# Optimization experiments

Hardware: AMD Instinct MI355X
Metric: run time of the kernel (lower is better)

## Reference

```python
import jax, jax.numpy as jnp
import numpy as np

M, N, L, D = 2048, 256, 128, 300  # context len, n entities, query len, d2
DROOT = float(np.sqrt(D))


def setup_inputs() -> dict:
    key = jax.random.key(0)
    ks = jax.random.split(key, 16)
    s = 0.05
    return {
        "context_emb": jax.random.normal(ks[0], (M, D), jnp.float32),
        "query_emb": jax.random.normal(ks[1], (L, D), jnp.float32),
        "bin_M": (jax.random.uniform(ks[2], (M, N)) < 0.02).astype(jnp.float32),  # sparse token->entity incidence
        "adj": (jax.random.uniform(ks[3], (N, N)) < 0.05).astype(jnp.float32),    # entity graph adjacency
        "V": jax.random.normal(ks[4], (D, 2 * D), jnp.float32) * s,
        "U": jax.random.normal(ks[5], (D, 2 * D), jnp.float32) * s,
        "b": jax.random.normal(ks[6], (D,), jnp.float32) * s,
        "W": jax.random.normal(ks[7], (2 * D,), jnp.float32) * s,
        "w_att": jax.random.normal(ks[8], (3, D), jnp.float32) * s,   # BiDAF trilinear weights (w_c, w_q, w_cq)
        "b_att": jax.random.normal(ks[9], (3,), jnp.float32) * s,
        "W_red": jax.random.normal(ks[10], (D, 4 * D), jnp.float32) * s,  # BiDAF reduction Linear(4*d2 -> d2)
        "b_red": jax.random.normal(ks[11], (D,), jnp.float32) * s,
        "W_ih": jax.random.normal(ks[12], (4 * D, 2 * D), jnp.float32) * s,  # LSTM input weights
        "b_ih": jax.random.normal(ks[13], (4 * D,), jnp.float32) * s,
        "b_hh": jax.random.normal(ks[14], (4 * D,), jnp.float32) * s,
        "passes": 1,
    }


def _tok2ent(context, bin_M):
    # avg_pool1d over full M divides by M (zeros of unmasked tokens included) -> exact mean/M
    mean = (bin_M.T @ context) / M                       # (N, D)
    masked = context[:, None, :] * bin_M[:, :, None]     # (M, N, D) dominant intermediate
    mx = masked.max(axis=0)                              # (N, D) max includes the zeros, as in torch
    return jnp.concatenate([mean, mx], axis=-1)          # (N, 2D)


def _graph_attention(ent, query, adj, V, U, b, W):
    q = query.mean(axis=0)                               # avg-pooled query (D,)
    gammas = ((q @ V) @ ent.T) / DROOT                   # (N,)
    E = jax.nn.sigmoid(gammas)[:, None] * ent            # soft entity mask, (N, 2D)
    hidden = E @ U.T + b                                 # (N, D)
    a_i = hidden @ W[:D]                                 # (N,) source half of W.[h_i;h_j]
    c_j = hidden @ W[D:]                                 # (N,)
    betas = jnp.where(adj > 0, jax.nn.leaky_relu(a_i[:, None] + c_j[None, :]), 0.0)
    # original exponentiates ALL betas incl. the zeros of non-edges -> plain softmax over axis 1
    alphas = jax.nn.softmax(betas, axis=1)               # (N, N)
    # E_t[i] = relu( sum_{j: adj[i,j]} alphas[j,i] * hidden[j] )
    return jax.nn.relu((adj * alphas.T) @ hidden)        # (N, D)


def _bidaf(ent, query, w_att, b_att, W_red, b_red):
    # trilinear similarity S[l, n] = w_c.q_l + w_q.e_n + w_cq.(q_l * e_n)
    S = (query @ w_att[0] + b_att[0])[:, None] \
        + (ent @ w_att[1] + b_att[1])[None, :] \
        + (query * w_att[2]) @ ent.T + b_att[2]          # (L, N)
    c2q = jax.nn.softmax(S, axis=1) @ ent                # (L, D)
    q2c = jax.nn.softmax(S.max(axis=1), axis=0) @ query  # (D,)
    x = jnp.concatenate([query, c2q, query * c2q, query * q2c[None, :]], axis=-1)  # (L, 4D)
    return x @ W_red.T + b_red                           # (L, D)


def _graph2doc(context, ent, bin_M, W_ih, b_ih, b_hh):
    x = jnp.concatenate([context, bin_M @ ent], axis=-1)  # (M, 2D)
    # nn.LSTM fed (seq=1, batch=M, 2D) from zero state == one LSTM-cell step per token
    gates = x @ W_ih.T + (b_ih + b_hh)                    # (M, 4D), torch gate order i,f,g,o
    i, f, g, o = jnp.split(gates, 4, axis=-1)
    c = jax.nn.sigmoid(i) * jnp.tanh(g)                   # f*c0 vanishes since c0 = 0
    return jax.nn.sigmoid(o) * jnp.tanh(c)                # (M, D)


def reference(context_emb, query_emb, bin_M, adj, V, U, b, W, w_att, b_att,
              W_red, b_red, W_ih, b_ih, b_hh, passes):
    ctx, qry = context_emb, query_emb
    for _ in range(passes):
        ent = _tok2ent(ctx, bin_M)                        # (N, 2D)
        E_t = _graph_attention(ent, qry, adj, V, U, b, W)  # (N, D)
        qry = _bidaf(E_t, qry, w_att, b_att, W_red, b_red)  # (L, D)
        ctx = _graph2doc(ctx, E_t, bin_M, W_ih, b_ih, b_hh)  # (M, D)
    return ctx, qry
```

## Files before the change

### kernel.cpp

```cpp
#include <hip/hip_runtime.h>
#include <hip/hip_bf16.h>
#include <math.h>

#define MM 2048
#define NN 256
#define LL 128
#define DD 300
#define D2 600
#define D4 1200
#define DROOT 17.320508075688775f

#define KP 608
#define NP 960
#define GM 64
#define GDT 64
#define GK 32

typedef __attribute__((ext_vector_type(8))) short bf16x8;
typedef __attribute__((ext_vector_type(4))) float f32x4;

__device__ __forceinline__ float sigmoidf_(float x) { return 1.f / (1.f + expf(-x)); }

__device__ __forceinline__ ushort f2bf(float v) {
    union { float f; unsigned u; } x; x.f = v;
    unsigned r = x.u + 0x7fffu + ((x.u >> 16) & 1u);
    return (ushort)(r >> 16);
}

__device__ __forceinline__ float dot4_(float4 a, float4 b) {
    return a.x * b.x + a.y * b.y + a.z * b.z + a.w * b.w;
}

__device__ __forceinline__ float bfdot8(uint4 u, float4 x0, float4 x1) {
    union { unsigned v; float f; } a, b;
    float s = 0.f;
    a.v = u.x << 16; b.v = u.x & 0xffff0000u; s += a.f * x0.x; s += b.f * x0.y;
    a.v = u.y << 16; b.v = u.y & 0xffff0000u; s += a.f * x0.z; s += b.f * x0.w;
    a.v = u.z << 16; b.v = u.z & 0xffff0000u; s += a.f * x1.x; s += b.f * x1.y;
    a.v = u.w << 16; b.v = u.w & 0xffff0000u; s += a.f * x1.z; s += b.f * x1.w;
    return s;
}

__device__ __forceinline__ float wave_red_sum(float v) {
    for (int off = 32; off; off >>= 1) v += __shfl_down(v, off);
    return v;
}

__global__ __launch_bounds__(256) void k_prep(const float* __restrict__ binM,
                                              const float* __restrict__ Wih,
                                              const float* __restrict__ U,
                                              const float* __restrict__ Wred,
                                              const float* __restrict__ query,
                                              const float* __restrict__ V,
                                              ushort* __restrict__ Wb,
                                              ushort* __restrict__ Ub,
                                              ushort* __restrict__ Wredb,
                                              unsigned* __restrict__ binMbits,
                                              float* __restrict__ qVp) {
    __shared__ float qp2[2][75];
    __shared__ float qp_s[75];
    int r = blockIdx.x, t = threadIdx.x;
    if (r < NP) {
        int s = r / 320, dd = r % 320;
        bool valid = (dd < DD);
        int src = (s == 0) ? dd : ((s == 1) ? 600 + dd : 900 + dd);
        for (int e = t; e < KP; e += 256) {
            float v = (valid && e < D2) ? Wih[(size_t)src * D2 + e] : 0.f;
            Wb[(size_t)r * KP + e] = f2bf(v);
        }
    } else if (r < NP + DD) {
        int rr = r - NP;
        for (int e = t; e < D2; e += 256) Ub[(size_t)rr * D2 + e] = f2bf(U[(size_t)rr * D2 + e]);
    } else if (r < NP + 2 * DD) {
        int rr = r - NP - DD;
        for (int e = t; e < D4; e += 256) Wredb[(size_t)rr * D4 + e] = f2bf(Wred[(size_t)rr * D4 + e]);
    } else if (r < NP + 2 * DD + 12) {
        int q = r - NP - 2 * DD;
        int kb = q >> 2, sl = q & 3;
        int dbase = sl * 75;
        if (t < 150) {
            int dd = t % 75, half = t / 75;
            float s = 0.f;
            #pragma unroll 8
            for (int l = half * 64; l < half * 64 + 64; ++l) s += query[l * DD + dbase + dd];
            qp2[half][dd] = s;
        }
        __syncthreads();
        if (t < 75) qp_s[t] = (qp2[0][t] + qp2[1][t]) * (1.f / LL);
        __syncthreads();
        int k = kb * 256 + t;
        if (k < D2) {
            float acc = 0.f;
            #pragma unroll 5
            for (int i = 0; i < 75; ++i) acc += qp_s[i] * V[(size_t)(dbase + i) * D2 + k];
            qVp[sl * D2 + k] = acc;
        }
    } else {
        int blk = r - NP - 2 * DD - 12;
        int m0 = blk * 32;
        unsigned mask = 0u;
        #pragma unroll 8
        for (int i = 0; i < 32; ++i) {
            if (binM[(size_t)(m0 + i) * NN + t] != 0.f) mask |= (1u << i);
        }
        binMbits[(size_t)t * 64 + blk] = mask;
    }
}

__global__ __launch_bounds__(960) void k_hidden(const float* __restrict__ ctx,
                                                const unsigned* __restrict__ binMbits,
                                                const float* __restrict__ qVp,
                                                const ushort* __restrict__ Ub,
                                                const float* __restrict__ bvec,
                                                const float* __restrict__ W,
                                                float* __restrict__ hidden,
                                                float* __restrict__ a_i,
                                                float* __restrict__ c_j) {
    __shared__ int lst[MM];
    __shared__ int wbase_s[65];
    __shared__ alignas(16) float e_s[D2];
    __shared__ float h_s[DD];
    __shared__ float red[2][16];
    __shared__ float sig_s;
    int n = blockIdx.x, t = threadIdx.x, wv = t >> 6, lane = t & 63;
    unsigned mword = (t < 64) ? binMbits[(size_t)n * 64 + t] : 0u;
    if (t < 64) wbase_s[t] = (int)__popc(mword);
    __syncthreads();
    if (t == 0) {
        int s = 0;
        for (int w = 0; w < 64; ++w) { int c = wbase_s[w]; wbase_s[w] = s; s += c; }
        wbase_s[64] = s;
    }
    __syncthreads();
    if (t < 64) {
        int base = wbase_s[t];
        unsigned x = mword;
        while (x) {
            int b = __ffs((int)x) - 1;
            lst[base++] = t * 32 + b;
            x &= x - 1;
        }
    }
    __syncthreads();
    int total = wbase_s[64];
    if (t < DD) {
        float sum = 0.f, mx = 0.f;
        int i = 0;
        for (; i + 4 <= total; i += 4) {
            float v0 = ctx[(size_t)lst[i] * DD + t];
            float v1 = ctx[(size_t)lst[i + 1] * DD + t];
            float v2 = ctx[(size_t)lst[i + 2] * DD + t];
            float v3 = ctx[(size_t)lst[i + 3] * DD + t];
            sum += v0; mx = fmaxf(mx, v0);
            sum += v1; mx = fmaxf(mx, v1);
            sum += v2; mx = fmaxf(mx, v2);
            sum += v3; mx = fmaxf(mx, v3);
        }
        for (; i < total; ++i) {
            float v = ctx[(size_t)lst[i] * DD + t];
            sum += v; mx = fmaxf(mx, v);
        }
        e_s[t]      = sum * (1.f / MM);
        e_s[DD + t] = mx;
    }
    __syncthreads();
    float part = 0.f;
    if (t < D2) part = e_s[t] * (qVp[t] + qVp[D2 + t] + qVp[2 * D2 + t] + qVp[3 * D2 + t]);
    part = wave_red_sum(part);
    if (lane == 0) red[0][wv] = part;
    __syncthreads();
    if (t == 0) {
        float s = 0.f;
        for (int w = 0; w < 15; ++w) s += red[0][w];
        sig_s = sigmoidf_(s / DROOT);
    }
    __syncthreads();
    float sg = sig_s;
    const float4* e4 = (const float4*)e_s;
    float4 ex0 = e4[2 * lane], ex1 = e4[2 * lane + 1];
    float4 ex2 = {0.f, 0.f, 0.f, 0.f}, ex3 = {0.f, 0.f, 0.f, 0.f};
    if (lane < 11) { ex2 = e4[128 + 2 * lane]; ex3 = e4[129 + 2 * lane]; }
    #pragma unroll 4
    for (int i = 0; i < 20; ++i) {
        int d = wv * 20 + i;
        const uint4* u4 = (const uint4*)(Ub + (size_t)d * D2);
        float p2 = bfdot8(u4[lane], ex0, ex1);
        if (lane < 11) p2 += bfdot8(u4[64 + lane], ex2, ex3);
        p2 = wave_red_sum(p2);
        if (lane == 0) {
            float h = sg * p2 + bvec[d];
            h_s[d] = h;
            hidden[n * DD + d] = h;
        }
    }
    __syncthreads();
    float wa = 0.f, wc = 0.f;
    if (t < DD) { float h = h_s[t]; wa = h * W[t]; wc = h * W[DD + t]; }
    wa = wave_red_sum(wa); wc = wave_red_sum(wc);
    if (lane == 0) { red[0][wv] = wa; red[1][wv] = wc; }
    __syncthreads();
    if (t == 0) {
        float A = 0.f, C = 0.f;
        for (int w = 0; w < 15; ++w) { A += red[0][w]; C += red[1][w]; }
        a_i[n] = A; c_j[n] = C;
    }
}

__global__ __launch_bounds__(256) void k_alphas(const float* __restrict__ adj,
                                                const float* __restrict__ ai,
                                                const float* __restrict__ cj,
                                                float* __restrict__ alphas) {
    __shared__ float red[4];
    __shared__ float bc[2];
    int i = blockIdx.x, j = threadIdx.x;
    float beta = 0.f;
    if (adj[i * NN + j] > 0.f) {
        float v = ai[i] + cj[j];
        beta = (v > 0.f) ? v : 0.01f * v;
    }
    float wm = beta;
    for (int off = 32; off; off >>= 1) wm = fmaxf(wm, __shfl_down(wm, off));
    if ((j & 63) == 0) red[j >> 6] = wm;
    __syncthreads();
    if (j == 0) bc[0] = fmaxf(fmaxf(red[0], red[1]), fmaxf(red[2], red[3]));
    __syncthreads();
    float e = expf(beta - bc[0]);
    float ws_ = e;
    for (int off = 32; off; off >>= 1) ws_ += __shfl_down(ws_, off);
    __syncthreads();
    if ((j & 63) == 0) red[j >> 6] = ws_;
    __syncthreads();
    if (j == 0) bc[1] = 1.f / (red[0] + red[1] + red[2] + red[3]);
    __syncthreads();
    alphas[i * NN + j] = e * bc[1];
}

__global__ __launch_bounds__(960) void k_Et(const float* __restrict__ adj,
                                            const float* __restrict__ alphas,
                                            const float* __restrict__ hidden,
                                            const float* __restrict__ w_att,
                                            const float* __restrict__ b_att,
                                            float* __restrict__ Et,
                                            float* __restrict__ EtT,
                                            float* __restrict__ ce) {
    __shared__ float w_s[NN];
    __shared__ float epart[3][DD];
    __shared__ float red[16];
    int i = blockIdx.x, t = threadIdx.x, wv = t >> 6;
    if (t < NN) w_s[t] = adj[i * NN + t] * alphas[t * NN + i];
    __syncthreads();
    int d = t % 320, sl = t / 320;
    int j0 = sl * 86, j1 = (sl == 2) ? NN : (j0 + 86);
    if (d < DD) {
        float acc = 0.f;
        #pragma unroll 2
        for (int j = j0; j < j1; ++j) acc += w_s[j] * hidden[(size_t)j * DD + d];
        epart[sl][d] = acc;
    }
    __syncthreads();
    float pv = 0.f;
    if (t < DD) {
        float etv = fmaxf(epart[0][t] + epart[1][t] + epart[2][t], 0.f);
        Et[i * DD + t] = etv;
        EtT[(size_t)t * NN + i] = etv;
        pv = etv * w_att[DD + t];
    }
    pv = wave_red_sum(pv);
    if ((t & 63) == 0) red[wv] = pv;
    __syncthreads();
    if (t == 0) {
        float s = 0.f;
        for (int w = 0; w < 15; ++w) s += red[w];
        ce[i] = s + b_att[1];
    }
}

__global__ __launch_bounds__(1024) void k_Bmid(const float* __restrict__ query,
                                               const float* __restrict__ Et,
                                               const float* __restrict__ EtT,
                                               const float* __restrict__ w_att,
                                               const float* __restrict__ b_att,
                                               const float* __restrict__ ce,
                                               const float* __restrict__ ctx,
                                               const float* __restrict__ binM,
                                               float* __restrict__ rowmax,
                                               float* __restrict__ c2qg,
                                               ushort* __restrict__ Xb) {
    __shared__ alignas(16) float qw[DD];
    __shared__ float s_row[NN];
    __shared__ alignas(16) float p_s[NN];
    __shared__ float red[16];
    __shared__ float cql_s, rmax_s, invs;
    __shared__ int lst4[4][NN];
    __shared__ int wcnt4[4][4];
    __shared__ int tot4[4];
    int t = threadIdx.x, wv = t >> 6, lane = t & 63;
    if (blockIdx.x < LL) {
        int l = blockIdx.x;
        float part = 0.f;
        if (t < DD) {
            float qv = query[l * DD + t];
            qw[t] = qv * w_att[2 * DD + t];
            part = qv * w_att[t];
        }
        part = wave_red_sum(part);
        if (lane == 0) red[wv] = part;
        __syncthreads();
        if (t == 0) {
            float s = 0.f;
            for (int w = 0; w < 16; ++w) s += red[w];
            cql_s = s + b_att[0];
        }
        __syncthreads();
        const float4* q4 = (const float4*)qw;
        float4 qb0 = q4[lane];
        float4 qb1 = (lane < 11) ? q4[64 + lane] : float4{0.f, 0.f, 0.f, 0.f};
        float wmax = -1e30f;
        #pragma unroll 4
        for (int i = 0; i < 16; ++i) {
            int n = wv * 16 + i;
            const float4* e4 = (const float4*)(Et + (size_t)n * DD);
            float4 a0 = e4[lane];
            float p2 = dot4_(a0, qb0);
            if (lane < 11) { float4 a1 = e4[64 + lane]; p2 += dot4_(a1, qb1); }
            p2 = wave_red_sum(p2);
            if (lane == 0) {
                float val = cql_s + ce[n] + p2 + b_att[2];
                s_row[n] = val;
                wmax = fmaxf(wmax, val);
            }
        }
        if (lane == 0) red[wv] = wmax;
        __syncthreads();
        if (t == 0) {
            float m = red[0];
            for (int w = 1; w < 16; ++w) m = fmaxf(m, red[w]);
            rmax_s = m;
            rowmax[l] = m;
        }
        __syncthreads();
        float e = 0.f;
        if (t < NN) e = expf(s_row[t] - rmax_s);
        float v = wave_red_sum(e);
        if (lane == 0) red[wv] = v;
        __syncthreads();
        if (t == 0) {
            float s = 0.f;
            for (int w = 0; w < 16; ++w) s += red[w];
            invs = 1.f / s;
        }
        __syncthreads();
        if (t < NN) p_s[t] = e * invs;
        __syncthreads();
        if (wv < 15) {
            const float4* p4 = (const float4*)p_s;
            float4 pb = p4[lane];
            #pragma unroll 4
            for (int i = 0; i < 20; ++i) {
                int d = wv * 20 + i;
                float4 a = ((const float4*)(EtT + (size_t)d * NN))[lane];
                float p2 = wave_red_sum(dot4_(a, pb));
                if (lane == 0) c2qg[l * DD + d] = p2;
            }
        }
    } else {
        int g = t >> 8, tt = t & 255;
        int w2 = tt >> 6;
        int m = (blockIdx.x - LL) * 4 + g;
        float b = binM[(size_t)m * NN + tt];
        unsigned long long mask = __ballot(b != 0.f);
        int prefix = __popcll(mask & ((1ull << lane) - 1ull));
        if (lane == 0) wcnt4[g][w2] = (int)__popcll(mask);
        __syncthreads();
        int wbase = 0;
        for (int w = 0; w < w2; ++w) wbase += wcnt4[g][w];
        if (b != 0.f) lst4[g][wbase + prefix] = tt;
        if (tt == 0) tot4[g] = wcnt4[g][0] + wcnt4[g][1] + wcnt4[g][2] + wcnt4[g][3];
        __syncthreads();
        int total = tot4[g];
        if (tt < 8) Xb[(size_t)m * KP + D2 + tt] = 0;
        for (int d = tt; d < DD; d += 256) {
            Xb[(size_t)m * KP + d] = f2bf(ctx[(size_t)m * DD + d]);
            float s = 0.f;
            for (int i = 0; i < total; ++i) s += Et[(size_t)lst4[g][i] * DD + d];
            Xb[(size_t)m * KP + DD + d] = f2bf(s);
        }
    }
}

__global__ __launch_bounds__(320) void k_tail(const float* __restrict__ c2qg,
                                              const float* __restrict__ rowmax,
                                              const float* __restrict__ query,
                                              const ushort* __restrict__ Wredb,
                                              const float* __restrict__ bred,
                                              const ushort* __restrict__ Xb,
                                              const ushort* __restrict__ Wb,
                                              const float* __restrict__ bih,
                                              const float* __restrict__ bhh,
                                              float* __restrict__ outq,
                                              float* __restrict__ outc) {
    __shared__ float pq[LL];
    __shared__ float q2c_s[DD];
    __shared__ alignas(16) float xs[D4];
    __shared__ float red[5];
    __shared__ float bc2[2];
    __shared__ ushort As[GM * GK];
    __shared__ ushort Bs[3][GDT * GK];
    int t = threadIdx.x, wv = t >> 6, lane = t & 63;
    if (blockIdx.x < 3 * LL) {
        int s = blockIdx.x / LL, l = blockIdx.x % LL;
        float v = (t < LL) ? rowmax[t] : -1e30f;
        float wm = v;
        for (int off = 32; off; off >>= 1) wm = fmaxf(wm, __shfl_down(wm, off));
        if (lane == 0) red[wv] = wm;
        __syncthreads();
        if (t == 0) {
            float m = red[0];
            for (int w = 1; w < 5; ++w) m = fmaxf(m, red[w]);
            bc2[0] = m;
        }
        __syncthreads();
        float e = (t < LL) ? expf(v - bc2[0]) : 0.f;
        float ws_ = wave_red_sum(e);
        __syncthreads();
        if (lane == 0) red[wv] = ws_;
        __syncthreads();
        if (t == 0) {
            float sm = 0.f;
            for (int w = 0; w < 5; ++w) sm += red[w];
            bc2[1] = 1.f / sm;
        }
        __syncthreads();
        if (t < LL) pq[t] = e * bc2[1];
        __syncthreads();
        if (t < DD) {
            float s2 = 0.f;
            #pragma unroll 4
            for (int l2 = 0; l2 < LL; ++l2) s2 += pq[l2] * query[l2 * DD + t];
            q2c_s[t] = s2;
        }
        __syncthreads();
        if (t < DD) {
            float c = c2qg[l * DD + t];
            float qv = query[l * DD + t];
            xs[t] = qv; xs[DD + t] = c; xs[2 * DD + t] = qv * c; xs[3 * DD + t] = qv * q2c_s[t];
        }
        __syncthreads();
        const float4* x4 = (const float4*)xs;
        float4 xb0 = x4[2 * lane], xb1 = x4[2 * lane + 1];
        float4 xb2 = x4[128 + 2 * lane], xb3 = x4[129 + 2 * lane];
        float4 xb4 = {0.f, 0.f, 0.f, 0.f}, xb5 = {0.f, 0.f, 0.f, 0.f};
        if (lane < 22) { xb4 = x4[256 + 2 * lane]; xb5 = x4[257 + 2 * lane]; }
        int d0 = s * 100 + wv * 20;
        #pragma unroll 2
        for (int i = 0; i < 20; ++i) {
            int d = d0 + i;
            const uint4* w4 = (const uint4*)(Wredb + (size_t)d * D4);
            float p2 = bfdot8(w4[lane], xb0, xb1) + bfdot8(w4[64 + lane], xb2, xb3);
            if (lane < 22) p2 += bfdot8(w4[128 + lane], xb4, xb5);
            p2 = wave_red_sum(p2);
            if (lane == 0) outq[l * DD + d] = bred[d] + p2;
        }
    } else {
        int g = blockIdx.x - 3 * LL;
        int m0 = (g & 31) * GM, d0 = (g >> 5) * GDT;
        int tid = t;
        int wm = wv >> 1, wn = wv & 1;
        int l15 = lane & 15, l4 = lane >> 4;
        f32x4 acc[3][2][2] = {};
        int srow = tid >> 2, kslot = tid & 3;
        int sidx = srow * GK + ((kslot ^ ((srow >> 1) & 3)) << 3);
        for (int k0 = 0; k0 < KP; k0 += GK) {
            if (tid < 256) {
                uint4 va = *(const uint4*)(Xb + (size_t)(m0 + srow) * KP + k0 + kslot * 8);
                *(uint4*)(As + sidx) = va;
                #pragma unroll
                for (int s = 0; s < 3; ++s) {
                    uint4 vb = *(const uint4*)(Wb + (size_t)(s * 320 + d0 + srow) * KP + k0 + kslot * 8);
                    *(uint4*)(Bs[s] + sidx) = vb;
                }
            }
            __syncthreads();
            if (tid < 256) {
                bf16x8 af[2], bfr[3][2];
                #pragma unroll
                for (int mi = 0; mi < 2; ++mi) {
                    int row = wm * 32 + mi * 16 + l15;
                    af[mi] = *(const bf16x8*)(As + row * GK + ((l4 ^ ((row >> 1) & 3)) << 3));
                }
                #pragma unroll
                for (int s = 0; s < 3; ++s)
                    #pragma unroll
                    for (int ni = 0; ni < 2; ++ni) {
                        int row = wn * 32 + ni * 16 + l15;
                        bfr[s][ni] = *(const bf16x8*)(Bs[s] + row * GK + ((l4 ^ ((row >> 1) & 3)) << 3));
                    }
                #pragma unroll
                for (int s = 0; s < 3; ++s)
                    #pragma unroll
                    for (int mi = 0; mi < 2; ++mi)
                        #pragma unroll
                        for (int ni = 0; ni < 2; ++ni)
                            acc[s][mi][ni] = __builtin_amdgcn_mfma_f32_16x16x32_bf16(af[mi], bfr[s][ni], acc[s][mi][ni], 0, 0, 0);
            }
            __syncthreads();
        }
        if (tid < 256) {
            #pragma unroll
            for (int mi = 0; mi < 2; ++mi) {
                #pragma unroll
                for (int ni = 0; ni < 2; ++ni) {
                    int d = d0 + wn * 32 + ni * 16 + l15;
                    if (d < DD) {
                        float bi = bih[d] + bhh[d];
                        float bg = bih[2 * DD + d] + bhh[2 * DD + d];
                        float bo = bih[3 * DD + d] + bhh[3 * DD + d];
                        int mrow = m0 + wm * 32 + mi * 16 + l4 * 4;
                        #pragma unroll
                        for (int r2 = 0; r2 < 4; ++r2) {
                            float gi = acc[0][mi][ni][r2] + bi;
                            float gg = acc[1][mi][ni][r2] + bg;
                            float go = acc[2][mi][ni][r2] + bo;
                            float c = sigmoidf_(gi) * tanhf(gg);
                            outc[(size_t)(mrow + r2) * DD + d] = sigmoidf_(go) * tanhf(c);
                        }
                    }
                }
            }
        }
    }
}

extern "C" void kernel_launch(void* const* d_in, const int* in_sizes, int n_in,
                              void* d_out, int out_size, void* d_ws, size_t ws_size,
                              hipStream_t stream) {
    const float* context = (const float*)d_in[0];
    const float* query   = (const float*)d_in[1];
    const float* binM    = (const float*)d_in[2];
    const float* adj     = (const float*)d_in[3];
    const float* V       = (const float*)d_in[4];
    const float* U       = (const float*)d_in[5];
    const float* bvec    = (const float*)d_in[6];
    const float* W       = (const float*)d_in[7];
    const float* w_att   = (const float*)d_in[8];
    const float* b_att   = (const float*)d_in[9];
    const float* W_red   = (const float*)d_in[10];
    const float* b_red   = (const float*)d_in[11];
    const float* W_ih    = (const float*)d_in[12];
    const float* b_ih    = (const float*)d_in[13];
    const float* b_hh    = (const float*)d_in[14];

    float* ws = (float*)d_ws;
    float* qVp    = ws;
    float* hidden = qVp    + 2400;
    float* a_i    = hidden + 76800;
    float* c_j    = a_i    + 256;
    float* alphas = c_j    + 256;
    float* Et     = alphas + 65536;
    float* EtT    = Et     + 76800;
    float* ce     = EtT    + 76800;
    float* rmax   = ce     + 256;
    float* c2qg   = rmax   + 128;
    unsigned* binMbits = (unsigned*)(c2qg + 38400);
    ushort* Xb    = (ushort*)(binMbits + (size_t)NN * 64);
    ushort* Wb    = Xb + (size_t)MM * KP;
    ushort* Ub    = Wb + (size_t)NP * KP;
    ushort* Wredb = Ub + (size_t)DD * D2;

    float* outc = (float*)d_out;
    float* outq = (float*)d_out + MM * DD;

    hipLaunchKernelGGL(k_prep,    dim3(NP + 2 * DD + 12 + 64), dim3(256), 0, stream,
                       binM, W_ih, U, W_red, query, V, Wb, Ub, Wredb, binMbits, qVp);
    hipLaunchKernelGGL(k_hidden,  dim3(NN), dim3(960), 0, stream, context, binMbits, qVp, Ub, bvec, W, hidden, a_i, c_j);
    hipLaunchKernelGGL(k_alphas,  dim3(NN), dim3(256), 0, stream, adj, a_i, c_j, alphas);
    hipLaunchKernelGGL(k_Et,      dim3(NN), dim3(960), 0, stream, adj, alphas, hidden, w_att, b_att, Et, EtT, ce);
    hipLaunchKernelGGL(k_Bmid,    dim3(LL + MM / 4), dim3(1024), 0, stream,
                       query, Et, EtT, w_att, b_att, ce, context, binM, rmax, c2qg, Xb);
    hipLaunchKernelGGL(k_tail,    dim3(3 * LL + 160), dim3(320), 0, stream,
                       c2qg, rmax, query, Wredb, b_red, Xb, Wb, b_ih, b_hh, outq, outc);
}
```

Baseline: 115.5 us.

## Fuse post-prep kernels into one cooperative persistent kernel with grid syncs

Replaces the hidden, alphas, Et, Bmid and tail kernels with a single cooperative kernel of 256 blocks of 1024 threads that moves between phases with grid.sync(). The alphas matrix is no longer materialized; per-row softmax statistics (mstat, rinv) are stored instead. The LSTM GEMM tiles are regrouped as four 256-thread sub-tiles per block. This removes several kernel launch gaps and intermediate round trips. In exchange the grid is capped at 256 blocks, uses a large shared-memory footprint, and pays grid-wide barrier costs. Phases that previously used more blocks may lose parallelism.

```diff
diff --git a/kernel.cpp b/kernel.cpp
--- a/kernel.cpp
+++ b/kernel.cpp
@@ -1,6 +1,9 @@
 #include <hip/hip_runtime.h>
+#include <hip/hip_cooperative_groups.h>
 #include <hip/hip_bf16.h>
 #include <math.h>
+
+namespace cg = cooperative_groups;
 
 #define MM 2048
 #define NN 256
@@ -107,331 +110,334 @@
     }
 }
 
-__global__ __launch_bounds__(960) void k_hidden(const float* __restrict__ ctx,
-                                                const unsigned* __restrict__ binMbits,
-                                                const float* __restrict__ qVp,
-                                                const ushort* __restrict__ Ub,
-                                                const float* __restrict__ bvec,
-                                                const float* __restrict__ W,
-                                                float* __restrict__ hidden,
-                                                float* __restrict__ a_i,
-                                                float* __restrict__ c_j) {
+__global__ __launch_bounds__(1024) void k_main(const float* __restrict__ ctx,
+                                               const float* __restrict__ binM,
+                                               const float* __restrict__ adj,
+                                               const float* __restrict__ query,
+                                               const float* __restrict__ qVp,
+                                               const unsigned* __restrict__ binMbits,
+                                               const ushort* __restrict__ Ub,
+                                               const ushort* __restrict__ Wredb,
+                                               const ushort* __restrict__ Wb,
+                                               const float* __restrict__ bvec,
+                                               const float* __restrict__ W,
+                                               const float* __restrict__ w_att,
+                                               const float* __restrict__ b_att,
+                                               const float* __restrict__ bred,
+                                               const float* __restrict__ bih,
+                                               const float* __restrict__ bhh,
+                                               float* __restrict__ hidden,
+                                               float* __restrict__ a_i,
+                                               float* __restrict__ c_j,
+                                               float* __restrict__ mstat,
+                                               float* __restrict__ rinv,
+                                               float* __restrict__ Et,
+                                               float* __restrict__ EtT,
+                                               float* __restrict__ ce,
+                                               float* __restrict__ rmax,
+                                               float* __restrict__ c2qg,
+                                               ushort* __restrict__ Xb,
+                                               float* __restrict__ outq,
+                                               float* __restrict__ outc) {
+    cg::grid_group grid = cg::this_grid();
     __shared__ int lst[MM];
     __shared__ int wbase_s[65];
     __shared__ alignas(16) float e_s[D2];
     __shared__ float h_s[DD];
-    __shared__ float red[2][16];
-    __shared__ float sig_s;
-    int n = blockIdx.x, t = threadIdx.x, wv = t >> 6, lane = t & 63;
-    unsigned mword = (t < 64) ? binMbits[(size_t)n * 64 + t] : 0u;
-    if (t < 64) wbase_s[t] = (int)__popc(mword);
-    __syncthreads();
-    if (t == 0) {
-        int s = 0;
-        for (int w = 0; w < 64; ++w) { int c = wbase_s[w]; wbase_s[w] = s; s += c; }
-        wbase_s[64] = s;
-    }
-    __syncthreads();
-    if (t < 64) {
-        int base = wbase_s[t];
-        unsigned x = mword;
-        while (x) {
-            int b = __ffs((int)x) - 1;
-            lst[base++] = t * 32 + b;
-            x &= x - 1;
-        }
-    }
-    __syncthreads();
-    int total = wbase_s[64];
-    if (t < DD) {
-        float sum = 0.f, mx = 0.f;
-        int i = 0;
-        for (; i + 4 <= total; i += 4) {
-            float v0 = ctx[(size_t)lst[i] * DD + t];
-            float v1 = ctx[(size_t)lst[i + 1] * DD + t];
-            float v2 = ctx[(size_t)lst[i + 2] * DD + t];
-            float v3 = ctx[(size_t)lst[i + 3] * DD + t];
-            sum += v0; mx = fmaxf(mx, v0);
-            sum += v1; mx = fmaxf(mx, v1);
-            sum += v2; mx = fmaxf(mx, v2);
-            sum += v3; mx = fmaxf(mx, v3);
-        }
-        for (; i < total; ++i) {
-            float v = ctx[(size_t)lst[i] * DD + t];
-            sum += v; mx = fmaxf(mx, v);
-        }
-        e_s[t]      = sum * (1.f / MM);
-        e_s[DD + t] = mx;
-    }
-    __syncthreads();
-    float part = 0.f;
-    if (t < D2) part = e_s[t] * (qVp[t] + qVp[D2 + t] + qVp[2 * D2 + t] + qVp[3 * D2 + t]);
-    part = wave_red_sum(part);
-    if (lane == 0) red[0][wv] = part;
-    __syncthreads();
-    if (t == 0) {
-        float s = 0.f;
-        for (int w = 0; w < 15; ++w) s += red[0][w];
-        sig_s = sigmoidf_(s / DROOT);
-    }
-    __syncthreads();
-    float sg = sig_s;
-    const float4* e4 = (const float4*)e_s;
-    float4 ex0 = e4[2 * lane], ex1 = e4[2 * lane + 1];
-    float4 ex2 = {0.f, 0.f, 0.f, 0.f}, ex3 = {0.f, 0.f, 0.f, 0.f};
-    if (lane < 11) { ex2 = e4[128 + 2 * lane]; ex3 = e4[129 + 2 * lane]; }
-    #pragma unroll 4
-    for (int i = 0; i < 20; ++i) {
-        int d = wv * 20 + i;
-        const uint4* u4 = (const uint4*)(Ub + (size_t)d * D2);
-        float p2 = bfdot8(u4[lane], ex0, ex1);
-        if (lane < 11) p2 += bfdot8(u4[64 + lane], ex2, ex3);
-        p2 = wave_red_sum(p2);
-        if (lane == 0) {
-            float h = sg * p2 + bvec[d];
-            h_s[d] = h;
-            hidden[n * DD + d] = h;
-        }
-    }
-    __syncthreads();
-    float wa = 0.f, wc = 0.f;
-    if (t < DD) { float h = h_s[t]; wa = h * W[t]; wc = h * W[DD + t]; }
-    wa = wave_red_sum(wa); wc = wave_red_sum(wc);
-    if (lane == 0) { red[0][wv] = wa; red[1][wv] = wc; }
-    __syncthreads();
-    if (t == 0) {
-        float A = 0.f, C = 0.f;
-        for (int w = 0; w < 15; ++w) { A += red[0][w]; C += red[1][w]; }
-        a_i[n] = A; c_j[n] = C;
-    }
-}
-
-__global__ __launch_bounds__(256) void k_alphas(const float* __restrict__ adj,
-                                                const float* __restrict__ ai,
-                                                const float* __restrict__ cj,
-                                                float* __restrict__ alphas) {
-    __shared__ float red[4];
-    __shared__ float bc[2];
-    int i = blockIdx.x, j = threadIdx.x;
-    float beta = 0.f;
-    if (adj[i * NN + j] > 0.f) {
-        float v = ai[i] + cj[j];
-        beta = (v > 0.f) ? v : 0.01f * v;
-    }
-    float wm = beta;
-    for (int off = 32; off; off >>= 1) wm = fmaxf(wm, __shfl_down(wm, off));
-    if ((j & 63) == 0) red[j >> 6] = wm;
-    __syncthreads();
-    if (j == 0) bc[0] = fmaxf(fmaxf(red[0], red[1]), fmaxf(red[2], red[3]));
-    __syncthreads();
-    float e = expf(beta - bc[0]);
-    float ws_ = e;
-    for (int off = 32; off; off >>= 1) ws_ += __shfl_down(ws_, off);
-    __syncthreads();
-    if ((j & 63) == 0) red[j >> 6] = ws_;
-    __syncthreads();
-    if (j == 0) bc[1] = 1.f / (red[0] + red[1] + red[2] + red[3]);
-    __syncthreads();
-    alphas[i * NN + j] = e * bc[1];
-}
-
-__global__ __launch_bounds__(960) void k_Et(const float* __restrict__ adj,
-                                            const float* __restrict__ alphas,
-                                            const float* __restrict__ hidden,
-                                            const float* __restrict__ w_att,
-                                            const float* __restrict__ b_att,
-                                            float* __restrict__ Et,
-                                            float* __restrict__ EtT,
-                                            float* __restrict__ ce) {
+    __shared__ float red2[2][16];
+    __shared__ float scal[4];
     __shared__ float w_s[NN];
     __shared__ float epart[3][DD];
-    __shared__ float red[16];
-    int i = blockIdx.x, t = threadIdx.x, wv = t >> 6;
-    if (t < NN) w_s[t] = adj[i * NN + t] * alphas[t * NN + i];
-    __syncthreads();
-    int d = t % 320, sl = t / 320;
-    int j0 = sl * 86, j1 = (sl == 2) ? NN : (j0 + 86);
-    if (d < DD) {
-        float acc = 0.f;
-        #pragma unroll 2
-        for (int j = j0; j < j1; ++j) acc += w_s[j] * hidden[(size_t)j * DD + d];
-        epart[sl][d] = acc;
-    }
-    __syncthreads();
-    float pv = 0.f;
-    if (t < DD) {
-        float etv = fmaxf(epart[0][t] + epart[1][t] + epart[2][t], 0.f);
-        Et[i * DD + t] = etv;
-        EtT[(size_t)t * NN + i] = etv;
-        pv = etv * w_att[DD + t];
-    }
-    pv = wave_red_sum(pv);
-    if ((t & 63) == 0) red[wv] = pv;
-    __syncthreads();
-    if (t == 0) {
-        float s = 0.f;
-        for (int w = 0; w < 15; ++w) s += red[w];
-        ce[i] = s + b_att[1];
-    }
-}
-
-__global__ __launch_bounds__(1024) void k_Bmid(const float* __restrict__ query,
-                                               const float* __restrict__ Et,
-                                               const float* __restrict__ EtT,
-                                               const float* __restrict__ w_att,
-                                               const float* __restrict__ b_att,
-                                               const float* __restrict__ ce,
-                                               const float* __restrict__ ctx,
-                                               const float* __restrict__ binM,
-                                               float* __restrict__ rowmax,
-                                               float* __restrict__ c2qg,
-                                               ushort* __restrict__ Xb) {
     __shared__ alignas(16) float qw[DD];
     __shared__ float s_row[NN];
     __shared__ alignas(16) float p_s[NN];
-    __shared__ float red[16];
-    __shared__ float cql_s, rmax_s, invs;
     __shared__ int lst4[4][NN];
     __shared__ int wcnt4[4][4];
     __shared__ int tot4[4];
-    int t = threadIdx.x, wv = t >> 6, lane = t & 63;
-    if (blockIdx.x < LL) {
-        int l = blockIdx.x;
+    __shared__ float pq[LL];
+    __shared__ float q2c_s[DD];
+    __shared__ alignas(16) float xs[D4];
+    __shared__ ushort As4[4][GM * GK];
+    __shared__ ushort Bs4[4][3][GDT * GK];
+
+    int bid = blockIdx.x, t = threadIdx.x, wv = t >> 6, lane = t & 63;
+
+    {
+        int n = bid;
+        unsigned mword = (t < 64) ? binMbits[(size_t)n * 64 + t] : 0u;
+        if (t < 64) wbase_s[t] = (int)__popc(mword);
+        __syncthreads();
+        if (t == 0) {
+            int s = 0;
+            for (int w = 0; w < 64; ++w) { int c = wbase_s[w]; wbase_s[w] = s; s += c; }
+            wbase_s[64] = s;
+        }
+        __syncthreads();
+        if (t < 64) {
+            int base = wbase_s[t];
+            unsigned x = mword;
+            while (x) {
+                int b2 = __ffs((int)x) - 1;
+                lst[base++] = t * 32 + b2;
+                x &= x - 1;
+            }
+        }
+        __syncthreads();
+        int total = wbase_s[64];
+        if (t < DD) {
+            float sum = 0.f, mx = 0.f;
+            int i = 0;
+            for (; i + 4 <= total; i += 4) {
+                float v0 = ctx[(size_t)lst[i] * DD + t];
+                float v1 = ctx[(size_t)lst[i + 1] * DD + t];
+                float v2 = ctx[(size_t)lst[i + 2] * DD + t];
+                float v3 = ctx[(size_t)lst[i + 3] * DD + t];
+                sum += v0; mx = fmaxf(mx, v0);
+                sum += v1; mx = fmaxf(mx, v1);
+                sum += v2; mx = fmaxf(mx, v2);
+                sum += v3; mx = fmaxf(mx, v3);
+            }
+            for (; i < total; ++i) {
+                float v = ctx[(size_t)lst[i] * DD + t];
+                sum += v; mx = fmaxf(mx, v);
+            }
+            e_s[t]      = sum * (1.f / MM);
+            e_s[DD + t] = mx;
+        }
+        __syncthreads();
         float part = 0.f;
-        if (t < DD) {
-            float qv = query[l * DD + t];
-            qw[t] = qv * w_att[2 * DD + t];
-            part = qv * w_att[t];
-        }
+        if (t < D2) part = e_s[t] * (qVp[t] + qVp[D2 + t] + qVp[2 * D2 + t] + qVp[3 * D2 + t]);
         part = wave_red_sum(part);
-        if (lane == 0) red[wv] = part;
+        if (lane == 0) red2[0][wv] = part;
         __syncthreads();
         if (t == 0) {
             float s = 0.f;
-            for (int w = 0; w < 16; ++w) s += red[w];
-            cql_s = s + b_att[0];
-        }
-        __syncthreads();
-        const float4* q4 = (const float4*)qw;
-        float4 qb0 = q4[lane];
-        float4 qb1 = (lane < 11) ? q4[64 + lane] : float4{0.f, 0.f, 0.f, 0.f};
-        float wmax = -1e30f;
-        #pragma unroll 4
-        for (int i = 0; i < 16; ++i) {
-            int n = wv * 16 + i;
-            const float4* e4 = (const float4*)(Et + (size_t)n * DD);
-            float4 a0 = e4[lane];
-            float p2 = dot4_(a0, qb0);
-            if (lane < 11) { float4 a1 = e4[64 + lane]; p2 += dot4_(a1, qb1); }
-            p2 = wave_red_sum(p2);
-            if (lane == 0) {
-                float val = cql_s + ce[n] + p2 + b_att[2];
-                s_row[n] = val;
-                wmax = fmaxf(wmax, val);
-            }
-        }
-        if (lane == 0) red[wv] = wmax;
-        __syncthreads();
-        if (t == 0) {
-            float m = red[0];
-            for (int w = 1; w < 16; ++w) m = fmaxf(m, red[w]);
-            rmax_s = m;
-            rowmax[l] = m;
-        }
-        __syncthreads();
-        float e = 0.f;
-        if (t < NN) e = expf(s_row[t] - rmax_s);
-        float v = wave_red_sum(e);
-        if (lane == 0) red[wv] = v;
-        __syncthreads();
-        if (t == 0) {
-            float s = 0.f;
-            for (int w = 0; w < 16; ++w) s += red[w];
-            invs = 1.f / s;
-        }
-        __syncthreads();
-        if (t < NN) p_s[t] = e * invs;
-        __syncthreads();
+            for (int w = 0; w < 16; ++w) s += red2[0][w];
+            scal[0] = sigmoidf_(s / DROOT);
+        }
+        __syncthreads();
+        float sg = scal[0];
+        const float4* e4 = (const float4*)e_s;
+        float4 ex0 = e4[2 * lane], ex1 = e4[2 * lane + 1];
+        float4 ex2 = {0.f, 0.f, 0.f, 0.f}, ex3 = {0.f, 0.f, 0.f, 0.f};
+        if (lane < 11) { ex2 = e4[128 + 2 * lane]; ex3 = e4[129 + 2 * lane]; }
         if (wv < 15) {
-            const float4* p4 = (const float4*)p_s;
-            float4 pb = p4[lane];
             #pragma unroll 4
             for (int i = 0; i < 20; ++i) {
                 int d = wv * 20 + i;
-                float4 a = ((const float4*)(EtT + (size_t)d * NN))[lane];
-                float p2 = wave_red_sum(dot4_(a, pb));
-                if (lane == 0) c2qg[l * DD + d] = p2;
-            }
-        }
-    } else {
-        int g = t >> 8, tt = t & 255;
-        int w2 = tt >> 6;
-        int m = (blockIdx.x - LL) * 4 + g;
-        float b = binM[(size_t)m * NN + tt];
-        unsigned long long mask = __ballot(b != 0.f);
-        int prefix = __popcll(mask & ((1ull << lane) - 1ull));
-        if (lane == 0) wcnt4[g][w2] = (int)__popcll(mask);
-        __syncthreads();
-        int wbase = 0;
-        for (int w = 0; w < w2; ++w) wbase += wcnt4[g][w];
-        if (b != 0.f) lst4[g][wbase + prefix] = tt;
-        if (tt == 0) tot4[g] = wcnt4[g][0] + wcnt4[g][1] + wcnt4[g][2] + wcnt4[g][3];
-        __syncthreads();
-        int total = tot4[g];
-        if (tt < 8) Xb[(size_t)m * KP + D2 + tt] = 0;
-        for (int d = tt; d < DD; d += 256) {
-            Xb[(size_t)m * KP + d] = f2bf(ctx[(size_t)m * DD + d]);
+                const uint4* u4 = (const uint4*)(Ub + (size_t)d * D2);
+                float p2 = bfdot8(u4[lane], ex0, ex1);
+                if (lane < 11) p2 += bfdot8(u4[64 + lane], ex2, ex3);
+                p2 = wave_red_sum(p2);
+                if (lane == 0) {
+                    float h = sg * p2 + bvec[d];
+                    h_s[d] = h;
+                    hidden[n * DD + d] = h;
+                }
+            }
+        }
+        __syncthreads();
+        float wa = 0.f, wc = 0.f;
+        if (t < DD) { float h = h_s[t]; wa = h * W[t]; wc = h * W[DD + t]; }
+        wa = wave_red_sum(wa); wc = wave_red_sum(wc);
+        if (lane == 0) { red2[0][wv] = wa; red2[1][wv] = wc; }
+        __syncthreads();
+        if (t == 0) {
+            float A = 0.f, C = 0.f;
+            for (int w = 0; w < 16; ++w) { A += red2[0][w]; C += red2[1][w]; }
+            a_i[n] = A; c_j[n] = C;
+        }
+    }
+    grid.sync();
+
+    {
+        int j = bid;
+        bool act = (t < NN);
+        float beta = 0.f;
+        if (act && adj[(size_t)j * NN + t] > 0.f) {
+            float v = a_i[j] + c_j[t];
+            beta = (v > 0.f) ? v : 0.01f * v;
+        }
+        float bm = act ? beta : -1e30f;
+        for (int off = 32; off; off >>= 1) bm = fmaxf(bm, __shfl_down(bm, off));
+        if (lane == 0) red2[0][wv] = bm;
+        __syncthreads();
+        if (t == 0) {
+            float m = red2[0][0];
+            for (int w = 1; w < 16; ++w) m = fmaxf(m, red2[0][w]);
+            scal[0] = m;
+        }
+        __syncthreads();
+        float e = act ? expf(beta - scal[0]) : 0.f;
+        float s1 = wave_red_sum(e);
+        if (lane == 0) red2[1][wv] = s1;
+        __syncthreads();
+        if (t == 0) {
             float s = 0.f;
-            for (int i = 0; i < total; ++i) s += Et[(size_t)lst4[g][i] * DD + d];
-            Xb[(size_t)m * KP + DD + d] = f2bf(s);
+            for (int w = 0; w < 16; ++w) s += red2[1][w];
+            mstat[j] = scal[0];
+            rinv[j] = 1.f / s;
         }
     }
-}
-
-__global__ __launch_bounds__(320) void k_tail(const float* __restrict__ c2qg,
-                                              const float* __restrict__ rowmax,
-                                              const float* __restrict__ query,
-                                              const ushort* __restrict__ Wredb,
-                                              const float* __restrict__ bred,
-                                              const ushort* __restrict__ Xb,
-                                              const ushort* __restrict__ Wb,
-                                              const float* __restrict__ bih,
-                                              const float* __restrict__ bhh,
-                                              float* __restrict__ outq,
-                                              float* __restrict__ outc) {
-    __shared__ float pq[LL];
-    __shared__ float q2c_s[DD];
-    __shared__ alignas(16) float xs[D4];
-    __shared__ float red[5];
-    __shared__ float bc2[2];
-    __shared__ ushort As[GM * GK];
-    __shared__ ushort Bs[3][GDT * GK];
-    int t = threadIdx.x, wv = t >> 6, lane = t & 63;
-    if (blockIdx.x < 3 * LL) {
-        int s = blockIdx.x / LL, l = blockIdx.x % LL;
-        float v = (t < LL) ? rowmax[t] : -1e30f;
+    grid.sync();
+
+    {
+        int i = bid;
+        if (t < NN) {
+            float aj  = adj[(size_t)i * NN + t];
+            float adT = adj[(size_t)t * NN + i];
+            float v = a_i[t] + c_j[i];
+            float beta = (adT > 0.f) ? ((v > 0.f) ? v : 0.01f * v) : 0.f;
+            w_s[t] = aj * expf(beta - mstat[t]) * rinv[t];
+        }
+        __syncthreads();
+        int d = t % 320, sl = t / 320;
+        if (sl < 3 && d < DD) {
+            int j0 = sl * 86, j1 = (sl == 2) ? NN : (j0 + 86);
+            float acc = 0.f;
+            #pragma unroll 2
+            for (int j = j0; j < j1; ++j) acc += w_s[j] * hidden[(size_t)j * DD + d];
+            epart[sl][d] = acc;
+        }
+        __syncthreads();
+        float pv = 0.f;
+        if (t < DD) {
+            float etv = fmaxf(epart[0][t] + epart[1][t] + epart[2][t], 0.f);
+            Et[i * DD + t] = etv;
+            EtT[(size_t)t * NN + i] = etv;
+            pv = etv * w_att[DD + t];
+        }
+        pv = wave_red_sum(pv);
+        if (lane == 0) red2[0][wv] = pv;
+        __syncthreads();
+        if (t == 0) {
+            float s = 0.f;
+            for (int w = 0; w < 16; ++w) s += red2[0][w];
+            ce[i] = s + b_att[1];
+        }
+    }
+    grid.sync();
+
+    for (int u = bid; u < LL + MM / 4; u += 256) {
+        __syncthreads();
+        if (u < LL) {
+            int l = u;
+            float part = 0.f;
+            if (t < DD) {
+                float qv = query[l * DD + t];
+                qw[t] = qv * w_att[2 * DD + t];
+                part = qv * w_att[t];
+            }
+            part = wave_red_sum(part);
+            if (lane == 0) red2[0][wv] = part;
+            __syncthreads();
+            if (t == 0) {
+                float s = 0.f;
+                for (int w = 0; w < 16; ++w) s += red2[0][w];
+                scal[0] = s + b_att[0];
+            }
+            __syncthreads();
+            const float4* q4 = (const float4*)qw;
+            float4 qb0 = q4[lane];
+            float4 qb1 = (lane < 11) ? q4[64 + lane] : float4{0.f, 0.f, 0.f, 0.f};
+            float wmax = -1e30f;
+            #pragma unroll 4
+            for (int i = 0; i < 16; ++i) {
+                int n = wv * 16 + i;
+                const float4* e4 = (const float4*)(Et + (size_t)n * DD);
+                float4 a0 = e4[lane];
+                float p2 = dot4_(a0, qb0);
+                if (lane < 11) { float4 a1 = e4[64 + lane]; p2 += dot4_(a1, qb1); }
+                p2 = wave_red_sum(p2);
+                if (lane == 0) {
+                    float val = scal[0] + ce[n] + p2 + b_att[2];
+                    s_row[n] = val;
+                    wmax = fmaxf(wmax, val);
+                }
+            }
+            if (lane == 0) red2[0][wv] = wmax;
+            __syncthreads();
+            if (t == 0) {
+                float m = red2[0][0];
+                for (int w = 1; w < 16; ++w) m = fmaxf(m, red2[0][w]);
+                scal[1] = m;
+                rmax[l] = m;
+            }
+            __syncthreads();
+            float e = 0.f;
+            if (t < NN) e = expf(s_row[t] - scal[1]);
+            float v1 = wave_red_sum(e);
+            if (lane == 0) red2[0][wv] = v1;
+            __syncthreads();
+            if (t == 0) {
+                float s = 0.f;
+                for (int w = 0; w < 16; ++w) s += red2[0][w];
+                scal[2] = 1.f / s;
+            }
+            __syncthreads();
+            if (t < NN) p_s[t] = e * scal[2];
+            __syncthreads();
+            if (wv < 15) {
+                const float4* p4 = (const float4*)p_s;
+                float4 pb = p4[lane];
+                #pragma unroll 4
+                for (int i = 0; i < 20; ++i) {
+                    int d = wv * 20 + i;
+                    float4 a = ((const float4*)(EtT + (size_t)d * NN))[lane];
+                    float p2 = wave_red_sum(dot4_(a, pb));
+                    if (lane == 0) c2qg[l * DD + d] = p2;
+                }
+            }
+        } else {
+            int g = t >> 8, tt = t & 255;
+            int w2 = tt >> 6;
+            int m = (u - LL) * 4 + g;
+            float b = binM[(size_t)m * NN + tt];
+            unsigned long long mask = __ballot(b != 0.f);
+            int prefix = __popcll(mask & ((1ull << lane) - 1ull));
+            if (lane == 0) wcnt4[g][w2] = (int)__popcll(mask);
+            __syncthreads();
+            int wbase = 0;
+            for (int w = 0; w < w2; ++w) wbase += wcnt4[g][w];
+            if (b != 0.f) lst4[g][wbase + prefix] = tt;
+            if (tt == 0) tot4[g] = wcnt4[g][0] + wcnt4[g][1] + wcnt4[g][2] + wcnt4[g][3];
+            __syncthreads();
+            int total = tot4[g];
+            if (tt < 8) Xb[(size_t)m * KP + D2 + tt] = 0;
+            for (int d = tt; d < DD; d += 256) {
+                Xb[(size_t)m * KP + d] = f2bf(ctx[(size_t)m * DD + d]);
+                float s = 0.f;
+                for (int i = 0; i < total; ++i) s += Et[(size_t)lst4[g][i] * DD + d];
+                Xb[(size_t)m * KP + DD + d] = f2bf(s);
+            }
+        }
+    }
+    grid.sync();
+
+    if (bid < LL) {
+        int l = bid;
+        float v = (t < LL) ? rmax[t] : -1e30f;
         float wm = v;
         for (int off = 32; off; off >>= 1) wm = fmaxf(wm, __shfl_down(wm, off));
-        if (lane == 0) red[wv] = wm;
-        __syncthreads();
-        if (t == 0) {
-            float m = red[0];
-            for (int w = 1; w < 5; ++w) m = fmaxf(m, red[w]);
-            bc2[0] = m;
-        }
-        __syncthreads();
-        float e = (t < LL) ? expf(v - bc2[0]) : 0.f;
-        float ws_ = wave_red_sum(e);
-        __syncthreads();
-        if (lane == 0) red[wv] = ws_;
+        if (lane == 0) red2[0][wv] = wm;
+        __syncthreads();
+        if (t == 0) {
+            float m = red2[0][0];
+            for (int w = 1; w < 16; ++w) m = fmaxf(m, red2[0][w]);
+            scal[0] = m;
+        }
+        __syncthreads();
+        float e = (t < LL) ? expf(v - scal[0]) : 0.f;
+        float s1 = wave_red_sum(e);
+        if (lane == 0) red2[1][wv] = s1;
         __syncthreads();
         if (t == 0) {
             float sm = 0.f;
-            for (int w = 0; w < 5; ++w) sm += red[w];
-            bc2[1] = 1.f / sm;
-        }
-        __syncthreads();
-        if (t < LL) pq[t] = e * bc2[1];
+            for (int w = 0; w < 16; ++w) sm += red2[1][w];
+            scal[1] = 1.f / sm;
+        }
+        __syncthreads();
+        if (t < LL) pq[t] = e * scal[1];
         __syncthreads();
         if (t < DD) {
             float s2 = 0.f;
@@ -451,79 +457,76 @@
         float4 xb2 = x4[128 + 2 * lane], xb3 = x4[129 + 2 * lane];
         float4 xb4 = {0.f, 0.f, 0.f, 0.f}, xb5 = {0.f, 0.f, 0.f, 0.f};
         if (lane < 22) { xb4 = x4[256 + 2 * lane]; xb5 = x4[257 + 2 * lane]; }
-        int d0 = s * 100 + wv * 20;
-        #pragma unroll 2
-        for (int i = 0; i < 20; ++i) {
-            int d = d0 + i;
-            const uint4* w4 = (const uint4*)(Wredb + (size_t)d * D4);
-            float p2 = bfdot8(w4[lane], xb0, xb1) + bfdot8(w4[64 + lane], xb2, xb3);
-            if (lane < 22) p2 += bfdot8(w4[128 + lane], xb4, xb5);
-            p2 = wave_red_sum(p2);
-            if (lane == 0) outq[l * DD + d] = bred[d] + p2;
-        }
-    } else {
-        int g = blockIdx.x - 3 * LL;
-        int m0 = (g & 31) * GM, d0 = (g >> 5) * GDT;
-        int tid = t;
-        int wm = wv >> 1, wn = wv & 1;
+        if (wv < 15) {
+            #pragma unroll 2
+            for (int i = 0; i < 20; ++i) {
+                int d = wv * 20 + i;
+                const uint4* w4 = (const uint4*)(Wredb + (size_t)d * D4);
+                float p2 = bfdot8(w4[lane], xb0, xb1) + bfdot8(w4[64 + lane], xb2, xb3);
+                if (lane < 22) p2 += bfdot8(w4[128 + lane], xb4, xb5);
+                p2 = wave_red_sum(p2);
+                if (lane == 0) outq[l * DD + d] = bred[d] + p2;
+            }
+        }
+    } else if (bid < LL + 40) {
+        int sub = t >> 8, tid2 = t & 255;
+        int tt2 = (bid - LL) * 4 + sub;
+        int m0 = (tt2 & 31) * GM, d0 = (tt2 >> 5) * GDT;
+        int wv2 = tid2 >> 6;
+        int wm2 = wv2 >> 1, wn2 = wv2 & 1;
         int l15 = lane & 15, l4 = lane >> 4;
         f32x4 acc[3][2][2] = {};
-        int srow = tid >> 2, kslot = tid & 3;
+        int srow = tid2 >> 2, kslot = tid2 & 3;
         int sidx = srow * GK + ((kslot ^ ((srow >> 1) & 3)) << 3);
+        ushort* As = As4[sub];
         for (int k0 = 0; k0 < KP; k0 += GK) {
-            if (tid < 256) {
-                uint4 va = *(const uint4*)(Xb + (size_t)(m0 + srow) * KP + k0 + kslot * 8);
-                *(uint4*)(As + sidx) = va;
-                #pragma unroll
-                for (int s = 0; s < 3; ++s) {
-                    uint4 vb = *(const uint4*)(Wb + (size_t)(s * 320 + d0 + srow) * KP + k0 + kslot * 8);
-                    *(uint4*)(Bs[s] + sidx) = vb;
-                }
-            }
-            __syncthreads();
-            if (tid < 256) {
-                bf16x8 af[2], bfr[3][2];
-                #pragma unroll
-                for (int mi = 0; mi < 2; ++mi) {
-                    int row = wm * 32 + mi * 16 + l15;
-                    af[mi] = *(const bf16x8*)(As + row * GK + ((l4 ^ ((row >> 1) & 3)) << 3));
-                }
-                #pragma unroll
-                for (int s = 0; s < 3; ++s)
-                    #pragma unroll
-                    for (int ni = 0; ni < 2; ++ni) {
-                        int row = wn * 32 + ni * 16 + l15;
-                        bfr[s][ni] = *(const bf16x8*)(Bs[s] + row * GK + ((l4 ^ ((row >> 1) & 3)) << 3));
-                    }
-                #pragma unroll
-                for (int s = 0; s < 3; ++s)
-                    #pragma unroll
-                    for (int mi = 0; mi < 2; ++mi)
-                        #pragma unroll
-                        for (int ni = 0; ni < 2; ++ni)
-                            acc[s][mi][ni] = __builtin_amdgcn_mfma_f32_16x16x32_bf16(af[mi], bfr[s][ni], acc[s][mi][ni], 0, 0, 0);
-            }
-            __syncthreads();
-        }
-        if (tid < 256) {
+            uint4 va = *(const uint4*)(Xb + (size_t)(m0 + srow) * KP + k0 + kslot * 8);
+            *(uint4*)(As + sidx) = va;
+            #pragma unroll
+            for (int s = 0; s < 3; ++s) {
+                uint4 vb = *(const uint4*)(Wb + (size_t)(s * 320 + d0 + srow) * KP + k0 + kslot * 8);
+                *(uint4*)(Bs4[sub][s] + sidx) = vb;
+            }
+            __syncthreads();
+            bf16x8 af[2], bfr[3][2];
             #pragma unroll
             for (int mi = 0; mi < 2; ++mi) {
+                int row = wm2 * 32 + mi * 16 + l15;
+                af[mi] = *(const bf16x8*)(As + row * GK + ((l4 ^ ((row >> 1) & 3)) << 3));
+            }
+            #pragma unroll
+            for (int s = 0; s < 3; ++s)
                 #pragma unroll
                 for (int ni = 0; ni < 2; ++ni) {
-                    int d = d0 + wn * 32 + ni * 16 + l15;
-                    if (d < DD) {
-                        float bi = bih[d] + bhh[d];
-                        float bg = bih[2 * DD + d] + bhh[2 * DD + d];
-                        float bo = bih[3 * DD + d] + bhh[3 * DD + d];
-                        int mrow = m0 + wm * 32 + mi * 16 + l4 * 4;
-                        #pragma unroll
-                        for (int r2 = 0; r2 < 4; ++r2) {
-                            float gi = acc[0][mi][ni][r2] + bi;
-                            float gg = acc[1][mi][ni][r2] + bg;
-                            float go = acc[2][mi][ni][r2] + bo;
-                            float c = sigmoidf_(gi) * tanhf(gg);
-                            outc[(size_t)(mrow + r2) * DD + d] = sigmoidf_(go) * tanhf(c);
-                        }
+                    int row = wn2 * 32 + ni * 16 + l15;
+                    bfr[s][ni] = *(const bf16x8*)(Bs4[sub][s] + row * GK + ((l4 ^ ((row >> 1) & 3)) << 3));
+                }
+            #pragma unroll
+            for (int s = 0; s < 3; ++s)
+                #pragma unroll
+                for (int mi = 0; mi < 2; ++mi)
+                    #pragma unroll
+                    for (int ni = 0; ni < 2; ++ni)
+                        acc[s][mi][ni] = __builtin_amdgcn_mfma_f32_16x16x32_bf16(af[mi], bfr[s][ni], acc[s][mi][ni], 0, 0, 0);
+            __syncthreads();
+        }
+        #pragma unroll
+        for (int mi = 0; mi < 2; ++mi) {
+            #pragma unroll
+            for (int ni = 0; ni < 2; ++ni) {
+                int d = d0 + wn2 * 32 + ni * 16 + l15;
+                if (d < DD) {
+                    float bi = bih[d] + bhh[d];
+                    float bg = bih[2 * DD + d] + bhh[2 * DD + d];
+                    float bo = bih[3 * DD + d] + bhh[3 * DD + d];
+                    int mrow = m0 + wm2 * 32 + mi * 16 + l4 * 4;
+                    #pragma unroll
+                    for (int r2 = 0; r2 < 4; ++r2) {
+                        float gi = acc[0][mi][ni][r2] + bi;
+                        float gg = acc[1][mi][ni][r2] + bg;
+                        float go = acc[2][mi][ni][r2] + bo;
+                        float c = sigmoidf_(gi) * tanhf(gg);
+                        outc[(size_t)(mrow + r2) * DD + d] = sigmoidf_(go) * tanhf(c);
                     }
                 }
             }
@@ -555,8 +558,9 @@
     float* hidden = qVp    + 2400;
     float* a_i    = hidden + 76800;
     float* c_j    = a_i    + 256;
-    float* alphas = c_j    + 256;
-    float* Et     = alphas + 65536;
+    float* mstat  = c_j    + 256;
+    float* rinv   = mstat  + 256;
+    float* Et     = rinv   + 256;
     float* EtT    = Et     + 76800;
     float* ce     = EtT    + 76800;
     float* rmax   = ce     + 256;
@@ -570,13 +574,17 @@
     float* outc = (float*)d_out;
     float* outq = (float*)d_out + MM * DD;
 
-    hipLaunchKernelGGL(k_prep,    dim3(NP + 2 * DD + 12 + 64), dim3(256), 0, stream,
+    hipLaunchKernelGGL(k_prep, dim3(NP + 2 * DD + 12 + 64), dim3(256), 0, stream,
                        binM, W_ih, U, W_red, query, V, Wb, Ub, Wredb, binMbits, qVp);
-    hipLaunchKernelGGL(k_hidden,  dim3(NN), dim3(960), 0, stream, context, binMbits, qVp, Ub, bvec, W, hidden, a_i, c_j);
-    hipLaunchKernelGGL(k_alphas,  dim3(NN), dim3(256), 0, stream, adj, a_i, c_j, alphas);
-    hipLaunchKernelGGL(k_Et,      dim3(NN), dim3(960), 0, stream, adj, alphas, hidden, w_att, b_att, Et, EtT, ce);
-    hipLaunchKernelGGL(k_Bmid,    dim3(LL + MM / 4), dim3(1024), 0, stream,
-                       query, Et, EtT, w_att, b_att, ce, context, binM, rmax, c2qg, Xb);
-    hipLaunchKernelGGL(k_tail,    dim3(3 * LL + 160), dim3(320), 0, stream,
-                       c2qg, rmax, query, Wredb, b_red, Xb, Wb, b_ih, b_hh, outq, outc);
-}
+
+    void* args[] = {
+        (void*)&context, (void*)&binM, (void*)&adj, (void*)&query, (void*)&qVp,
+        (void*)&binMbits, (void*)&Ub, (void*)&Wredb, (void*)&Wb,
+        (void*)&bvec, (void*)&W, (void*)&w_att, (void*)&b_att, (void*)&b_red,
+        (void*)&b_ih, (void*)&b_hh,
+        (void*)&hidden, (void*)&a_i, (void*)&c_j, (void*)&mstat, (void*)&rinv,
+        (void*)&Et, (void*)&EtT, (void*)&ce, (void*)&rmax, (void*)&c2qg,
+        (void*)&Xb, (void*)&outq, (void*)&outc
+    };
+    hipLaunchCooperativeKernel((const void*)k_main, dim3(256), dim3(1024), args, 0, stream);
+}
```

After: 238.6 us. 107% more time.
